# Performance work log

Hardware: AMD Instinct MI355X
Metric: run time of the kernel (lower is better)

Reference implementation:

```python
import jax, jax.numpy as jnp
import numpy as np

NUM_CODEBOOKS = 2
CODEBOOK_SIZE = 256
OUT_GROUP = 1
IN_GROUP = 8
IN_FEATURES = 4096
OUT_FEATURES = 11008


def setup_inputs() -> dict:
    key = jax.random.key(0)
    k1, k2, k3, k4, k5 = jax.random.split(key, 5)
    num_out_groups = OUT_FEATURES // OUT_GROUP
    num_in_groups = IN_FEATURES // IN_GROUP
    x = jax.random.normal(k1, (4, 2048, IN_FEATURES), dtype=jnp.float32)
    codes = jax.random.randint(k2, (num_out_groups, num_in_groups, NUM_CODEBOOKS), 0, CODEBOOK_SIZE, dtype=jnp.int32)
    codebooks = jax.random.normal(k3, (NUM_CODEBOOKS, CODEBOOK_SIZE, OUT_GROUP, IN_GROUP), dtype=jnp.float32) * 0.05
    scales = jax.random.uniform(k4, (num_out_groups, 1, 1, 1), dtype=jnp.float32)
    bias = jax.random.normal(k5, (OUT_FEATURES,), dtype=jnp.float32)
    return {"x": x, "codes": codes, "codebooks": codebooks, "scales": scales, "bias": bias}


def _dequantize_weight(codes, codebooks, scales):
    # codes: [Og, Ig, C] int; codebooks: [C, K, og, ig]; scales: [Og,1,1,1]
    C = codebooks.shape[0]
    og, ig = codebooks.shape[2], codebooks.shape[3]
    Og, Ig = codes.shape[0], codes.shape[1]
    # gather per-codebook vectors: result [Og, Ig, C, og, ig]
    w = codebooks[jnp.arange(C)[None, None, :], codes]
    w = w.sum(axis=2)                      # [Og, Ig, og, ig] (additive quantization)
    w = w * scales                         # broadcast [Og,1,1,1]
    w = w.transpose(0, 2, 1, 3)            # [Og, og, Ig, ig]
    return w.reshape(Og * og, Ig * ig)     # [out_features, in_features]


def reference(x, codes, codebooks, scales, bias):
    W = _dequantize_weight(codes, codebooks, scales)
    return jnp.einsum('bsi,oi->bso', x, W) + bias
```

## Files before the change

### kernel.cpp

```cpp
#include <hip/hip_runtime.h>
#include <hip/hip_bf16.h>
#include <stdint.h>

#define IN_F 4096
#define OUT_F 11008
#define M_ROWS 8192
#define NIG 512
#define CBSZ 256

typedef _Float16 f16x8 __attribute__((ext_vector_type(8)));
typedef float f32x4 __attribute__((ext_vector_type(4)));

__global__ __launch_bounds__(256) void dequant_w_kernel(
    const int* __restrict__ codes, const float* __restrict__ cbs,
    _Float16* __restrict__ W)
{
  const int idx = blockIdx.x * 256 + threadIdx.x;
  const int2 c = ((const int2*)codes)[idx];
  const float4* e0 = (const float4*)(cbs + (size_t)c.x * 8);
  const float4* e1 = (const float4*)(cbs + (size_t)CBSZ * 8 + (size_t)c.y * 8);
  const float4 a0 = e0[0], a1 = e0[1];
  const float4 b0 = e1[0], b1 = e1[1];
  f16x8 w;
  w[0] = (_Float16)(a0.x + b0.x);
  w[1] = (_Float16)(a0.y + b0.y);
  w[2] = (_Float16)(a0.z + b0.z);
  w[3] = (_Float16)(a0.w + b0.w);
  w[4] = (_Float16)(a1.x + b1.x);
  w[5] = (_Float16)(a1.y + b1.y);
  w[6] = (_Float16)(a1.z + b1.z);
  w[7] = (_Float16)(a1.w + b1.w);
  *(f16x8*)(W + (size_t)idx * 8) = w;
}

__global__ __launch_bounds__(256) void convert_x_kernel(
    const float* __restrict__ x, _Float16* __restrict__ X)
{
  const size_t i = ((size_t)blockIdx.x * 256 + threadIdx.x) * 8;
  const float4 a = *(const float4*)(x + i);
  const float4 b = *(const float4*)(x + i + 4);
  f16x8 v;
  v[0] = (_Float16)a.x; v[1] = (_Float16)a.y;
  v[2] = (_Float16)a.z; v[3] = (_Float16)a.w;
  v[4] = (_Float16)b.x; v[5] = (_Float16)b.y;
  v[6] = (_Float16)b.z; v[7] = (_Float16)b.w;
  *(f16x8*)(X + i) = v;
}

#define BM 256
#define BN 256
#define BK 64
#define NKT (IN_F / BK)
#define GRID_MT (M_ROWS / BM)
#define GRID_NT (OUT_F / BN)

__global__ __launch_bounds__(512, 2) void gemm_pipe(
    const _Float16* __restrict__ X, const _Float16* __restrict__ Wd,
    const float* __restrict__ scales, const float* __restrict__ bias,
    float* __restrict__ out)
{
  __shared__ char smem[131072];

  const int cpx = (GRID_MT * GRID_NT) >> 3;
  const int wg = (blockIdx.x & 7) * cpx + (blockIdx.x >> 3);
  const int mt = wg & (GRID_MT - 1), nt = wg >> 5;
  const int m0 = mt * BM, n0 = nt * BN;

  const int t_ = threadIdx.x;
  const int wave = t_ >> 6, lane = t_ & 63;
  const int wm = wave >> 2, wn = wave & 3;
  const int r16 = lane & 15;
  const int q = lane >> 4;
  const int sw = r16 & 7;
  const int c0 = ((q ^ sw) << 4);
  const int c1 = (((4 | q) ^ sw) << 4);

  const int s_row0 = t_ >> 3;
  const int s_col  = (((t_ & 7) ^ ((t_ >> 3) & 7)) << 3);
  const _Float16* asrc = X  + (size_t)(m0 + s_row0) * IN_F + s_col;
  const _Float16* bsrc = Wd + (size_t)(n0 + s_row0) * IN_F + s_col;
  const int s_dst = wave * 1024;

  f32x4 acc[8][4] = {};
  f16x8 al0[4], al1[4], ah0[4], ah1[4];
  f16x8 bl0[2][2], bl1[2], bh0[2], bh1[2];

#define GLD(gsrc, ldst) __builtin_amdgcn_global_load_lds(                     \
    (const __attribute__((address_space(1))) void*)(gsrc),                    \
    (__attribute__((address_space(3))) void*)(ldst), 16, 0, 0)
#define STAGE_A(kt, bufc, i) GLD(asrc + (size_t)(kt) * BK + (size_t)(i) * 64 * IN_F, \
    smem + (bufc) * 65536 + (i) * 8192 + s_dst)
#define STAGE_B(kt, bufc, i) GLD(bsrc + (size_t)(kt) * BK + (size_t)(i) * 64 * IN_F, \
    smem + (bufc) * 65536 + 32768 + (i) * 8192 + s_dst)

#define RD_A(bufp, mm, cc) (*(const f16x8*)((bufp) + ((wm * 128 + (mm) * 16 + r16) << 7) + (cc)))
#define RD_B(bufp, nn, cc) (*(const f16x8*)((bufp) + 32768 + ((wn * 64 + (nn) * 16 + r16) << 7) + (cc)))

#define BAR   __builtin_amdgcn_s_barrier()
#define PRIO1 __builtin_amdgcn_s_setprio(1)
#define PRIO0 __builtin_amdgcn_s_setprio(0)
#define VM4 asm volatile("s_waitcnt vmcnt(4)" ::: "memory")
#define VM2 asm volatile("s_waitcnt vmcnt(2)" ::: "memory")
#define VM0 asm volatile("s_waitcnt vmcnt(0)" ::: "memory")

#define MG(AF, BF, MO, NO)                                                    \
    _Pragma("unroll")                                                         \
    for (int m = 0; m < 4; ++m)                                               \
      _Pragma("unroll")                                                       \
      for (int n = 0; n < 2; ++n)                                             \
        acc[(MO) + m][(NO) + n] = __builtin_amdgcn_mfma_f32_16x16x32_f16(     \
            AF[m], BF[n], acc[(MO) + m][(NO) + n], 0, 0, 0)

#define TILE(P, tt, SA, SB, GB, GA) do {                                      \
    char* bufT = smem + (P) * 65536;                                          \
    char* bufN = smem + (1 - (P)) * 65536;                                    \
                                                                      \
    if (SA) { STAGE_A((tt) + 1, 1 - (P), 0); STAGE_A((tt) + 1, 1 - (P), 1); } \
    _Pragma("unroll")                                                         \
    for (int m = 0; m < 4; ++m) al1[m] = RD_A(bufT, m, c1);                   \
    PRIO1; MG(al0, bl0[P], 0, 0); PRIO0; BAR;                                 \
                                                                      \
    if (SA) { STAGE_A((tt) + 1, 1 - (P), 2); STAGE_A((tt) + 1, 1 - (P), 3); } \
    _Pragma("unroll")                                                         \
    for (int n = 0; n < 2; ++n) bh1[n] = RD_B(bufT, 2 + n, c1);               \
    PRIO1; MG(al1, bl1, 0, 0); PRIO0; BAR;                                    \
                                                                      \
    _Pragma("unroll")                                                         \
    for (int n = 0; n < 2; ++n) bh0[n] = RD_B(bufT, 2 + n, c0);               \
    PRIO1; MG(al1, bh1, 0, 2); PRIO0; BAR;                                    \
                                                                      \
    _Pragma("unroll")                                                         \
    for (int m = 0; m < 4; ++m) ah0[m] = RD_A(bufT, 4 + m, c0);               \
    PRIO1; MG(al0, bh0, 0, 2); PRIO0; BAR;                                    \
                                                                      \
    _Pragma("unroll")                                                         \
    for (int m = 0; m < 4; ++m) ah1[m] = RD_A(bufT, 4 + m, c1);               \
    PRIO1; MG(ah0, bh0, 4, 2); PRIO0; BAR;                                    \
                                                                      \
    PRIO1; MG(ah1, bh1, 4, 2); PRIO0;                                         \
    if (GB) { VM4; }                                                          \
    BAR;                                                                      \
                                                                      \
    if (SB) { STAGE_B((tt) + 2, P, 0); STAGE_B((tt) + 2, P, 1); }             \
    _Pragma("unroll")                                                         \
    for (int n = 0; n < 2; ++n) bl0[1 - (P)][n] = RD_B(bufN, n, c0);          \
    PRIO1; MG(ah1, bl1, 4, 0); PRIO0;                                         \
    if ((GA) == 2) { VM2; }                                                   \
    if ((GA) == 0) { VM0; }                                                   \
    BAR;                                                                      \
                                                                      \
    if (SB) { STAGE_B((tt) + 2, P, 2); STAGE_B((tt) + 2, P, 3); }             \
    _Pragma("unroll")                                                         \
    for (int m = 0; m < 4; ++m) al0[m] = RD_A(bufN, m, c0);                   \
    _Pragma("unroll")                                                         \
    for (int n = 0; n < 2; ++n) bl1[n] = RD_B(bufN, n, c1);                   \
    PRIO1; MG(ah0, bl0[P], 4, 0); PRIO0; BAR;                                 \
  } while (0)

  {
    _Pragma("unroll")
    for (int i = 0; i < 4; ++i) { STAGE_A(0, 0, i); }
    _Pragma("unroll")
    for (int i = 0; i < 4; ++i) { STAGE_B(0, 0, i); }
    _Pragma("unroll")
    for (int i = 0; i < 4; ++i) { STAGE_B(1, 1, i); }
    VM4;
    BAR;
    char* buf0p = smem;
    _Pragma("unroll")
    for (int n = 0; n < 2; ++n) bl0[0][n] = RD_B(buf0p, n, c0);
    _Pragma("unroll")
    for (int n = 0; n < 2; ++n) bl1[n] = RD_B(buf0p, n, c1);
    _Pragma("unroll")
    for (int m = 0; m < 4; ++m) al0[m] = RD_A(buf0p, m, c0);
  }

  #pragma unroll 1
  for (int t = 0; t < 62; t += 2) {
    TILE(0, t,     1, 1, 1, 2);
    TILE(1, t + 1, 1, 1, 1, 2);
  }
  TILE(0, 62, 1, 0, 1, 0);
  TILE(1, 63, 0, 0, 0, -1);

  const int crow = (lane >> 4) << 2;
  #pragma unroll
  for (int nf = 0; nf < 4; ++nf) {
    const int col = n0 + wn * 64 + nf * 16 + r16;
    const float s = scales[col];
    const float bb = bias[col];
    #pragma unroll
    for (int mf = 0; mf < 8; ++mf) {
      const int rb = m0 + wm * 128 + mf * 16 + crow;
      #pragma unroll
      for (int r = 0; r < 4; ++r)
        out[(size_t)(rb + r) * OUT_F + col] = acc[mf][nf][r] * s + bb;
    }
  }
#undef TILE
#undef MG
#undef RD_A
#undef RD_B
#undef STAGE_A
#undef STAGE_B
#undef GLD
}

__global__ __launch_bounds__(256) void naive_kernel(
    const float* __restrict__ x, const int* __restrict__ codes,
    const float* __restrict__ cbs, const float* __restrict__ scales,
    const float* __restrict__ bias, float* __restrict__ out)
{
  __shared__ float xrow[IN_F];
  const int m = blockIdx.x;
  for (int i = threadIdx.x; i < IN_F; i += 256)
    xrow[i] = x[(size_t)m * IN_F + i];
  __syncthreads();
  for (int o = threadIdx.x; o < OUT_F; o += 256) {
    float acc = 0.f;
    const int2* crow = (const int2*)codes + (size_t)o * NIG;
    for (int g = 0; g < NIG; ++g) {
      const int2 c = crow[g];
      const float* e0 = cbs + (size_t)c.x * 8;
      const float* e1 = cbs + (size_t)CBSZ * 8 + (size_t)c.y * 8;
      const float* xr = xrow + g * 8;
      #pragma unroll
      for (int j = 0; j < 8; ++j) acc += (e0[j] + e1[j]) * xr[j];
    }
    out[(size_t)m * OUT_F + o] = acc * scales[o] + bias[o];
  }
}

extern "C" void kernel_launch(void* const* d_in, const int* in_sizes, int n_in,
                              void* d_out, int out_size, void* d_ws, size_t ws_size,
                              hipStream_t stream) {
  const float* x      = (const float*)d_in[0];
  const int*   codes  = (const int*)d_in[1];
  const float* cbs    = (const float*)d_in[2];
  const float* scales = (const float*)d_in[3];
  const float* bias   = (const float*)d_in[4];
  float* out = (float*)d_out;

  const size_t W_BYTES = (size_t)OUT_F * IN_F * sizeof(_Float16);
  const size_t X_BYTES = (size_t)M_ROWS * IN_F * sizeof(_Float16);

  if (ws_size < W_BYTES + X_BYTES) {
    naive_kernel<<<M_ROWS, 256, 0, stream>>>(x, codes, cbs, scales, bias, out);
    return;
  }

  _Float16* W = (_Float16*)d_ws;
  _Float16* X = (_Float16*)((char*)d_ws + W_BYTES);

  dequant_w_kernel<<<(OUT_F * NIG) / 256, 256, 0, stream>>>(codes, cbs, W);
  convert_x_kernel<<<(M_ROWS * IN_F / 8) / 256, 256, 0, stream>>>(x, X);
  gemm_pipe<<<GRID_MT * GRID_NT, 512, 0, stream>>>(X, W, scales, bias, out);
}
```

Baseline: 799.4 us.

## Restructure GEMM main loop into four-phase schedule with two-tile-ahead A prefetch

Replaces the eight-phase per-tile schedule with a four-phase one. Each phase loads both k-halves of a fragment group together and issues 16 MFMAs between barriers. A tiles are now prefetched two iterations ahead, like B, instead of one, and the prologue stages A for tile 1. The aim is fewer barriers per tile and more latency hiding for global-to-LDS loads, at the cost of more live fragment registers and reworked vmcnt waits that must match the new issue order.

```diff
diff --git a/kernel.cpp b/kernel.cpp
--- a/kernel.cpp
+++ b/kernel.cpp
@@ -83,7 +83,7 @@
 
   f32x4 acc[8][4] = {};
   f16x8 al0[4], al1[4], ah0[4], ah1[4];
-  f16x8 bl0[2][2], bl1[2], bh0[2], bh1[2];
+  f16x8 bl0[2][2], bl1[2][2], bh0[2], bh1[2];
 
 #define GLD(gsrc, ldst) __builtin_amdgcn_global_load_lds(                     \
     (const __attribute__((address_space(1))) void*)(gsrc),                    \
@@ -99,6 +99,7 @@
 #define BAR   __builtin_amdgcn_s_barrier()
 #define PRIO1 __builtin_amdgcn_s_setprio(1)
 #define PRIO0 __builtin_amdgcn_s_setprio(0)
+#define VM8 asm volatile("s_waitcnt vmcnt(8)" ::: "memory")
 #define VM4 asm volatile("s_waitcnt vmcnt(4)" ::: "memory")
 #define VM2 asm volatile("s_waitcnt vmcnt(2)" ::: "memory")
 #define VM0 asm volatile("s_waitcnt vmcnt(0)" ::: "memory")
@@ -111,50 +112,38 @@
         acc[(MO) + m][(NO) + n] = __builtin_amdgcn_mfma_f32_16x16x32_f16(     \
             AF[m], BF[n], acc[(MO) + m][(NO) + n], 0, 0, 0)
 
-#define TILE(P, tt, SA, SB, GB, GA) do {                                      \
+#define TILE4(P, tt, SB, SA, GP2, GP3) do {                                   \
     char* bufT = smem + (P) * 65536;                                          \
     char* bufN = smem + (1 - (P)) * 65536;                                    \
-                                                                      \
-    if (SA) { STAGE_A((tt) + 1, 1 - (P), 0); STAGE_A((tt) + 1, 1 - (P), 1); } \
-    _Pragma("unroll")                                                         \
-    for (int m = 0; m < 4; ++m) al1[m] = RD_A(bufT, m, c1);                   \
-    PRIO1; MG(al0, bl0[P], 0, 0); PRIO0; BAR;                                 \
-                                                                      \
-    if (SA) { STAGE_A((tt) + 1, 1 - (P), 2); STAGE_A((tt) + 1, 1 - (P), 3); } \
-    _Pragma("unroll")                                                         \
-    for (int n = 0; n < 2; ++n) bh1[n] = RD_B(bufT, 2 + n, c1);               \
-    PRIO1; MG(al1, bl1, 0, 0); PRIO0; BAR;                                    \
-                                                                      \
-    _Pragma("unroll")                                                         \
-    for (int n = 0; n < 2; ++n) bh0[n] = RD_B(bufT, 2 + n, c0);               \
-    PRIO1; MG(al1, bh1, 0, 2); PRIO0; BAR;                                    \
-                                                                      \
-    _Pragma("unroll")                                                         \
-    for (int m = 0; m < 4; ++m) ah0[m] = RD_A(bufT, 4 + m, c0);               \
-    PRIO1; MG(al0, bh0, 0, 2); PRIO0; BAR;                                    \
-                                                                      \
-    _Pragma("unroll")                                                         \
-    for (int m = 0; m < 4; ++m) ah1[m] = RD_A(bufT, 4 + m, c1);               \
-    PRIO1; MG(ah0, bh0, 4, 2); PRIO0; BAR;                                    \
-                                                                      \
-    PRIO1; MG(ah1, bh1, 4, 2); PRIO0;                                         \
-    if (GB) { VM4; }                                                          \
+             \
+    _Pragma("unroll")                                                         \
+    for (int n = 0; n < 2; ++n) { bh0[n] = RD_B(bufT, 2 + n, c0);             \
+                                  bh1[n] = RD_B(bufT, 2 + n, c1); }           \
+    PRIO1; MG(al0, bl0[P], 0, 0); MG(al1, bl1[P], 0, 0); PRIO0; BAR;          \
+                                            \
+    _Pragma("unroll")                                                         \
+    for (int m = 0; m < 4; ++m) { ah0[m] = RD_A(bufT, 4 + m, c0);             \
+                                  ah1[m] = RD_A(bufT, 4 + m, c1); }           \
+    PRIO1; MG(al0, bh0, 0, 2); MG(al1, bh1, 0, 2); PRIO0;                     \
+    if (GP2) { VM2; }                                                         \
     BAR;                                                                      \
-                                                                      \
-    if (SB) { STAGE_B((tt) + 2, P, 0); STAGE_B((tt) + 2, P, 1); }             \
-    _Pragma("unroll")                                                         \
-    for (int n = 0; n < 2; ++n) bl0[1 - (P)][n] = RD_B(bufN, n, c0);          \
-    PRIO1; MG(ah1, bl1, 4, 0); PRIO0;                                         \
-    if ((GA) == 2) { VM2; }                                                   \
-    if ((GA) == 0) { VM0; }                                                   \
+          \
+    if (SB) { STAGE_B((tt) + 2, P, 0); STAGE_B((tt) + 2, P, 1);               \
+              STAGE_B((tt) + 2, P, 2); STAGE_B((tt) + 2, P, 3); }             \
+    _Pragma("unroll")                                                         \
+    for (int m = 0; m < 4; ++m) { al0[m] = RD_A(bufN, m, c0);                 \
+                                  al1[m] = RD_A(bufN, m, c1); }               \
+    PRIO1; MG(ah0, bh0, 4, 2); MG(ah1, bh1, 4, 2); PRIO0;                     \
+    if ((GP3) == 2) { VM4; }                                                  \
+    if ((GP3) == 0) { VM0; }                                                  \
     BAR;                                                                      \
-                                                                      \
-    if (SB) { STAGE_B((tt) + 2, P, 2); STAGE_B((tt) + 2, P, 3); }             \
-    _Pragma("unroll")                                                         \
-    for (int m = 0; m < 4; ++m) al0[m] = RD_A(bufN, m, c0);                   \
-    _Pragma("unroll")                                                         \
-    for (int n = 0; n < 2; ++n) bl1[n] = RD_B(bufN, n, c1);                   \
-    PRIO1; MG(ah0, bl0[P], 4, 0); PRIO0; BAR;                                 \
+                                                         \
+    if (SA) { STAGE_A((tt) + 2, P, 0); STAGE_A((tt) + 2, P, 2);               \
+              STAGE_A((tt) + 2, P, 1); STAGE_A((tt) + 2, P, 3); }             \
+    _Pragma("unroll")                                                         \
+    for (int n = 0; n < 2; ++n) { bl0[1 - (P)][n] = RD_B(bufN, n, c0);        \
+                                  bl1[1 - (P)][n] = RD_B(bufN, n, c1); }      \
+    PRIO1; MG(ah0, bl0[P], 4, 0); MG(ah1, bl1[P], 4, 0); PRIO0; BAR;          \
   } while (0)
 
   {
@@ -164,24 +153,25 @@
     for (int i = 0; i < 4; ++i) { STAGE_B(0, 0, i); }
     _Pragma("unroll")
     for (int i = 0; i < 4; ++i) { STAGE_B(1, 1, i); }
-    VM4;
+    STAGE_A(1, 1, 0); STAGE_A(1, 1, 2); STAGE_A(1, 1, 1); STAGE_A(1, 1, 3);
+    VM8;
     BAR;
     char* buf0p = smem;
     _Pragma("unroll")
-    for (int n = 0; n < 2; ++n) bl0[0][n] = RD_B(buf0p, n, c0);
-    _Pragma("unroll")
-    for (int n = 0; n < 2; ++n) bl1[n] = RD_B(buf0p, n, c1);
-    _Pragma("unroll")
-    for (int m = 0; m < 4; ++m) al0[m] = RD_A(buf0p, m, c0);
+    for (int m = 0; m < 4; ++m) { al0[m] = RD_A(buf0p, m, c0);
+                                  al1[m] = RD_A(buf0p, m, c1); }
+    _Pragma("unroll")
+    for (int n = 0; n < 2; ++n) { bl0[0][n] = RD_B(buf0p, n, c0);
+                                  bl1[0][n] = RD_B(buf0p, n, c1); }
   }
 
   #pragma unroll 1
   for (int t = 0; t < 62; t += 2) {
-    TILE(0, t,     1, 1, 1, 2);
-    TILE(1, t + 1, 1, 1, 1, 2);
-  }
-  TILE(0, 62, 1, 0, 1, 0);
-  TILE(1, 63, 0, 0, 0, -1);
+    TILE4(0, t,     1, 1, 1, 2);
+    TILE4(1, t + 1, 1, 1, 1, 2);
+  }
+  TILE4(0, 62, 0, 0, 1, 0);
+  TILE4(1, 63, 0, 0, 0, -1);
 
   const int crow = (lane >> 4) << 2;
   #pragma unroll
@@ -197,7 +187,7 @@
         out[(size_t)(rb + r) * OUT_F + col] = acc[mf][nf][r] * s + bb;
     }
   }
-#undef TILE
+#undef TILE4
 #undef MG
 #undef RD_A
 #undef RD_B
```

Result: slower. 1.544 ms (+93.2%).
